# Performance work log

Hardware: AMD Instinct MI355X
Metric: run time of the kernel (lower is better)

## Reference

```python
import jax, jax.numpy as jnp
import numpy as np

M = 16
C = 7 * M          # 112, stage-8 channels
CLS = 20
TOPK = 3
NQ = 20000         # current-frame active sites at stage 8
NS = 8192          # support-frame active sites at stage 8
SCALE = 128.0      # voxel coordinate range at this depth


def setup_inputs() -> dict:
    key = jax.random.key(0)
    ks = jax.random.split(key, 9)
    coords_q = jax.random.uniform(ks[0], (NQ, 3), jnp.float32) * SCALE
    coords_s = jax.random.uniform(ks[1], (NS, 3), jnp.float32) * SCALE
    x7 = jax.random.normal(ks[2], (NQ, C), jnp.float32)
    feat_s7 = jax.random.normal(ks[3], (NS, C), jnp.float32)
    feat_s = jax.random.normal(ks[4], (NS, C), jnp.float32)
    w_attn = jax.random.normal(ks[5], (C,), jnp.float32) * 0.1
    W1 = jax.random.normal(ks[6], (2 * C, C), jnp.float32) * (1.0 / np.sqrt(2 * C))
    gamma = jnp.ones((C,), jnp.float32)
    beta = jnp.zeros((C,), jnp.float32)
    W2 = jax.random.normal(ks[7], (C, C), jnp.float32) * (1.0 / np.sqrt(C))
    W_cls = jax.random.normal(ks[8], (C, CLS), jnp.float32) * (1.0 / np.sqrt(C))
    b_cls = jnp.zeros((CLS,), jnp.float32)
    return dict(coords_q=coords_q, coords_s=coords_s, x7=x7, feat_s7=feat_s7,
                feat_s=feat_s, w_attn=w_attn, W1=W1, gamma=gamma, beta=beta,
                W2=W2, W_cls=W_cls, b_cls=b_cls)


def reference(coords_q, coords_s, x7, feat_s7, feat_s, w_attn, W1, gamma, beta, W2, W_cls, b_cls):
    # GlobalMeanAttentionPooling: attention-weighted mean over support sites -> global vector [C]
    a = jax.nn.softmax(feat_s7 @ w_attn)          # [NS]
    g = a @ feat_s7                                # [C]
    # GlobalMaskLayer: channel-wise sigmoid gating of current-frame features
    feat_q = x7 * jax.nn.sigmoid(g)                # [NQ, C]
    # DistMatchLayer_v4: top-3 nearest support voxels per query, softmax(-d2) weighting
    q2 = jnp.sum(coords_q * coords_q, -1, keepdims=True)   # [NQ, 1]
    s2 = jnp.sum(coords_s * coords_s, -1)                  # [NS]
    d2 = q2 + s2[None, :] - 2.0 * (coords_q @ coords_s.T)  # [NQ, NS]
    negd, idx = jax.lax.top_k(-d2, TOPK)                   # [NQ, K]
    w = jax.nn.softmax(negd, axis=-1)                      # [NQ, K]
    matched = jnp.einsum('nk,nkc->nc', w, feat_s[idx])     # [NQ, C]
    # tune_sub: 1x1 subconv (14m->7m) -> BN(eval affine) + ReLU -> 1x1 subconv (7m->7m)
    h = jnp.concatenate([feat_q, matched], -1) @ W1        # [NQ, C]
    h = jax.nn.relu(h * gamma + beta) @ W2                 # [NQ, C]
    # final classifier linear
    return h @ W_cls + b_cls                               # [NQ, CLS]
```

## Files before the change

### kernel.cpp

```cpp
#include <hip/hip_runtime.h>

#define NQv 20000
#define NSv 8192
#define Cv  112
#define CLSv 20
#define INFF 3.4e38f
#define JINF 0x7fffffff

#define GC 16
#define NCELL 4096
#define CELLH 8.0f
#define INVH 0.125f

#define POOLB 32
#define PT 256
#define PNW (POOLB * PT / 64)

#define SBLK (NQv / 4)
#define MB (NQv / 32)
#define WS_START 3616
#define WS_PTS4  5668
#define WS_W1TH  38440
#define WS_W1TL  50984
#define WS_W2TH  63528
#define WS_W2TL  70696
#define WS_WCT   77864

typedef __attribute__((ext_vector_type(8))) short bf16x8;
typedef __attribute__((ext_vector_type(4))) float f32x4;
typedef unsigned short us;

__device__ __forceinline__ float bf2f(us u) {
    union { unsigned int i; float f; } v; v.i = ((unsigned int)u) << 16; return v.f;
}
__device__ __forceinline__ us f2bf(float f) {
    union { float f; unsigned int i; } v; v.f = f;
    unsigned int r = v.i + 0x7fffu + ((v.i >> 16) & 1u);
    return (us)(r >> 16);
}
__device__ __forceinline__ void split(float v, us& h, us& l) {
    h = f2bf(v); l = f2bf(v - bf2f(h));
}

__global__ __launch_bounds__(PT) void k_prep(const float* __restrict__ cs,
                                             const float* __restrict__ fs7,
                                             const float* __restrict__ wat,
                                             const float* __restrict__ W1,
                                             const float* __restrict__ W2,
                                             const float* __restrict__ Wc,
                                             float* __restrict__ ws) {
    int b = blockIdx.x, tid = threadIdx.x;

    if (b == POOLB + 1) {
        us* w1h = (us*)(ws + WS_W1TH);
        us* w1l = (us*)(ws + WS_W1TL);
        for (int idx = tid; idx < Cv * 224; idx += PT) {
            int c = idx / 224, k = idx - c * 224;
            us h, l; split(W1[k * Cv + c], h, l);
            w1h[c * 224 + k] = h; w1l[c * 224 + k] = l;
        }
        return;
    }
    if (b == POOLB + 2) {
        us* w2h = (us*)(ws + WS_W2TH);
        us* w2l = (us*)(ws + WS_W2TL);
        for (int idx = tid; idx < Cv * 128; idx += PT) {
            int c = idx >> 7, k = idx & 127;
            float v = (k < Cv) ? W2[k * Cv + c] : 0.f;
            us h, l; split(v, h, l);
            w2h[c * 128 + k] = h; w2l[c * 128 + k] = l;
        }
        float* wct = ws + WS_WCT;
        for (int idx = tid; idx < CLSv * Cv; idx += PT) {
            int cls = idx / Cv, k = idx - cls * Cv;
            wct[cls * Cv + k] = Wc[k * CLSv + cls];
        }
        return;
    }
    if (b == POOLB) {
        __shared__ int cnt[NCELL];
        __shared__ int ssum[PT];
        us* startg = (us*)(ws + WS_START);
        float4* pts4 = (float4*)(ws + WS_PTS4);
        for (int i = tid; i < NCELL; i += PT) cnt[i] = 0;
        __syncthreads();
        for (int k = 0; k < NSv / PT; ++k) {
            int p = k * PT + tid;
            float x = cs[3 * p], y = cs[3 * p + 1], z = cs[3 * p + 2];
            int cx = (int)(x * INVH), cy = (int)(y * INVH), cz = (int)(z * INVH);
            cx = cx > 15 ? 15 : cx; cy = cy > 15 ? 15 : cy; cz = cz > 15 ? 15 : cz;
            atomicAdd(&cnt[(cz * GC + cy) * GC + cx], 1);
        }
        __syncthreads();
        int base = tid * 16, local = 0, c[16];
        #pragma unroll
        for (int i = 0; i < 16; ++i) { c[i] = cnt[base + i]; local += c[i]; }
        ssum[tid] = local;
        __syncthreads();
        for (int off = 1; off < PT; off <<= 1) {
            int v = (tid >= off) ? ssum[tid - off] : 0;
            __syncthreads();
            ssum[tid] += v;
            __syncthreads();
        }
        int run = ssum[tid] - local;
        #pragma unroll
        for (int i = 0; i < 16; ++i) {
            startg[base + i] = (us)run;
            cnt[base + i] = run;
            run += c[i];
        }
        if (tid == 0) startg[NCELL] = (us)NSv;
        __syncthreads();
        for (int k = 0; k < NSv / PT; ++k) {
            int p = k * PT + tid;
            float x = cs[3 * p], y = cs[3 * p + 1], z = cs[3 * p + 2];
            int cx = (int)(x * INVH), cy = (int)(y * INVH), cz = (int)(z * INVH);
            cx = cx > 15 ? 15 : cx; cy = cy > 15 ? 15 : cy; cz = cz > 15 ? 15 : cz;
            int slot = atomicAdd(&cnt[(cz * GC + cy) * GC + cx], 1);
            pts4[slot] = make_float4(-2.f * x, -2.f * y, -2.f * z, (float)p);
        }
        return;
    }

    __shared__ float red[PT / 64][Cv + 1];
    int gtid = b * PT + tid;
    int wid = gtid >> 6, lw = tid >> 6, lane = gtid & 63, l2 = lane * 2;
    float2 wa = make_float2(0.f, 0.f);
    if (lane < 56) wa = *(const float2*)(wat + l2);
    float gx = 0.f, gy = 0.f, z = 0.f;
    for (int g = 0; g < 8; ++g) {
        float2 f[8]; float part[8];
        #pragma unroll
        for (int u = 0; u < 8; ++u) {
            int i = wid + (g * 8 + u) * PNW;
            f[u] = (lane < 56) ? *(const float2*)(fs7 + i * Cv + l2) : make_float2(0.f, 0.f);
            part[u] = f[u].x * wa.x + f[u].y * wa.y;
        }
        #pragma unroll
        for (int off = 32; off; off >>= 1)
            #pragma unroll
            for (int u = 0; u < 8; ++u) part[u] += __shfl_xor(part[u], off, 64);
        #pragma unroll
        for (int u = 0; u < 8; ++u) {
            float p = __expf(part[u]);
            gx = fmaf(p, f[u].x, gx); gy = fmaf(p, f[u].y, gy); z += p;
        }
    }
    if (lane < 56) { red[lw][l2] = gx; red[lw][l2 + 1] = gy; }
    if (lane == 0) red[lw][Cv] = z;
    __syncthreads();
    if (tid < Cv + 1)
        ws[b * (Cv + 1) + tid] = red[0][tid] + red[1][tid] + red[2][tid] + red[3][tid];
}

__device__ __forceinline__ void scan_run(const float4* __restrict__ pts4,
                                         int a, int b, float qx, float qy, float qz,
                                         float& E0, float& E1, float& E2,
                                         int& J0, int& J1, int& J2) {
    for (int k = a; k < b; ++k) {
        float4 P = pts4[k];
        float x = -0.5f * P.x, y = -0.5f * P.y, z = -0.5f * P.z;
        float s2 = fmaf(x, x, fmaf(y, y, z * z));
        float e = fmaf(qx, P.x, fmaf(qy, P.y, fmaf(qz, P.z, s2)));
        int j = (int)P.w;
        bool lt2 = (e < E2) || (e == E2 && j < J2);
        if (lt2) {
            bool lt1 = (e < E1) || (e == E1 && j < J1);
            bool lt0 = (e < E0) || (e == E0 && j < J0);
            E2 = lt1 ? E1 : e;              J2 = lt1 ? J1 : j;
            E1 = lt0 ? E0 : (lt1 ? e : E1); J1 = lt0 ? J0 : (lt1 ? j : J1);
            if (lt0) { E0 = e; J0 = j; }
        }
    }
}

__global__ __launch_bounds__(256) void k_search(const float* __restrict__ cq,
                                                const float* __restrict__ ws,
                                                float* __restrict__ out) {
    const us* __restrict__ startg = (const us*)(ws + WS_START);
    const float4* __restrict__ pts4 = (const float4*)(ws + WS_PTS4);
    int tid = threadIdx.x, lane = tid & 63, widx = tid >> 6;
    int q = blockIdx.x * 4 + widx;
    float qx = cq[3 * q], qy = cq[3 * q + 1], qz = cq[3 * q + 2];
    float q2 = fmaf(qx, qx, fmaf(qy, qy, qz * qz));
    int cx = (int)(qx * INVH), cy = (int)(qy * INVH), cz = (int)(qz * INVH);
    cx = cx > 15 ? 15 : cx; cy = cy > 15 ? 15 : cy; cz = cz > 15 ? 15 : cz;
    float E0 = INFF, E1 = INFF, E2 = INFF;
    int   J0 = JINF, J1 = JINF, J2 = JINF;

    if (lane < 27) {
        int dz = lane / 9 - 1, dy = (lane / 3) % 3 - 1, dx = lane % 3 - 1;
        int xc = cx + dx, yc = cy + dy, zc = cz + dz;
        if ((unsigned)xc < 16u && (unsigned)yc < 16u && (unsigned)zc < 16u) {
            int cc = (zc * GC + yc) * GC + xc;
            scan_run(pts4, startg[cc], startg[cc + 1], qx, qy, qz, E0, E1, E2, J0, J1, J2);
        }
    }
    for (int s = 2; s <= 15; ++s) {
        float t0 = E0, t1 = E1, t2 = E2;
        #pragma unroll
        for (int off = 1; off < 64; off <<= 1) {
            float b0 = __shfl_xor(t0, off, 64);
            float b1 = __shfl_xor(t1, off, 64);
            float b2 = __shfl_xor(t2, off, 64);
            float xx = fmaxf(t0, b0), yy = fminf(t1, b1);
            float zz = fmaxf(t1, b1), uu = fminf(t2, b2);
            t0 = fminf(t0, b0);
            t1 = fminf(xx, yy);
            t2 = fminf(fminf(fmaxf(xx, yy), zz), uu);
        }
        int r = s - 1;
        int xl = cx - r > 0 ? cx - r : 0, xh = cx + r < 15 ? cx + r : 15;
        int yl = cy - r > 0 ? cy - r : 0, yh = cy + r < 15 ? cy + r : 15;
        int zl = cz - r > 0 ? cz - r : 0, zh = cz + r < 15 ? cz + r : 15;
        float fx = INFF, fy = INFF, fz = INFF;
        if (xl > 0)  fx = qx - xl * CELLH;
        if (xh < 15) fx = fminf(fx, (xh + 1) * CELLH - qx);
        if (yl > 0)  fy = qy - yl * CELLH;
        if (yh < 15) fy = fminf(fy, (yh + 1) * CELLH - qy);
        if (zl > 0)  fz = qz - zl * CELLH;
        if (zh < 15) fz = fminf(fz, (zh + 1) * CELLH - qz);
        float dmin = fminf(fx, fminf(fy, fz));
        if (dmin * dmin > t2 + q2 + 0.5f) break;

        int side = 2 * s + 1, s2n = side * side, tot = s2n * side;
        for (int idx = lane; idx < tot; idx += 64) {
            int dz = idx / s2n - s;
            int rem = idx - (dz + s) * s2n;
            int dy = rem / side - s;
            int dx = rem - (dy + s) * side - s;
            int ax = dx < 0 ? -dx : dx, ay = dy < 0 ? -dy : dy, az = dz < 0 ? -dz : dz;
            if (ax != s && ay != s && az != s) continue;
            int xc = cx + dx, yc = cy + dy, zc = cz + dz;
            if ((unsigned)xc > 15u || (unsigned)yc > 15u || (unsigned)zc > 15u) continue;
            int cc = (zc * GC + yc) * GC + xc;
            scan_run(pts4, startg[cc], startg[cc + 1], qx, qy, qz, E0, E1, E2, J0, J1, J2);
        }
    }
    float h0 = E0, h1 = E1, h2 = E2; int g0 = J0, g1 = J1, g2 = J2;
    float EF[3]; int JF[3];
    #pragma unroll
    for (int t = 0; t < 3; ++t) {
        float mv = h0; int mj = g0;
        #pragma unroll
        for (int off = 1; off < 64; off <<= 1) {
            float ov = __shfl_xor(mv, off, 64);
            int   oj = __shfl_xor(mj, off, 64);
            if (ov < mv || (ov == mv && oj < mj)) { mv = ov; mj = oj; }
        }
        EF[t] = mv; JF[t] = mj;
        bool win = (h0 == mv) && (g0 == mj);
        h0 = win ? h1 : h0; g0 = win ? g1 : g0;
        h1 = win ? h2 : h1; g1 = win ? g2 : g1;
        h2 = win ? INFF : h2; g2 = win ? JINF : g2;
    }
    if (lane == 0) {
        int A0 = (JF[0] < 0 || JF[0] >= NSv) ? 0 : JF[0];
        int A1 = (JF[1] < 0 || JF[1] >= NSv) ? 0 : JF[1];
        int A2 = (JF[2] < 0 || JF[2] >= NSv) ? 0 : JF[2];
        ((int*)out)[q * CLSv]     = A0 | (A1 << 16);
        ((int*)out)[q * CLSv + 1] = A2;
    }
}

__global__ __launch_bounds__(448) void k_mlp(
        const float* __restrict__ cq, const float* __restrict__ cs,
        const float* __restrict__ x7, const float* __restrict__ fs,
        const float* __restrict__ gma, const float* __restrict__ bta,
        const float* __restrict__ bc, const float* __restrict__ ws,
        float* __restrict__ out) {
    __shared__ __align__(16) us vbh[32 * 232];
    __shared__ __align__(16) us vbl[32 * 232];
    __shared__ __align__(16) us hbh[32 * 136];
    __shared__ __align__(16) us hbl[32 * 136];
    __shared__ __align__(16) float h2f[32 * 116];
    __shared__ float gate[Cv];
    __shared__ int   qi[32][3];
    __shared__ float qw[32][3];

    int tid = threadIdx.x;
    int q0 = blockIdx.x * 32;

    if (tid < Cv) {
        float st = 0.f, zt = 0.f;
        for (int b = 0; b < POOLB; ++b) {
            st += ws[b * (Cv + 1) + tid];
            zt += ws[b * (Cv + 1) + Cv];
        }
        gate[tid] = 1.0f / (1.0f + __expf(-(st / zt)));
    }
    int ut = tid - 128;
    if (ut >= 0 && ut < 32) {
        int q = q0 + ut;
        int A = ((const int*)out)[q * CLSv];
        int B = ((const int*)out)[q * CLSv + 1];
        int J0 = A & 0xFFFF, J1 = (A >> 16) & 0xFFFF, J2 = B;
        J0 = (J0 < 0 || J0 >= NSv) ? 0 : J0;
        J1 = (J1 < 0 || J1 >= NSv) ? 0 : J1;
        J2 = (J2 < 0 || J2 >= NSv) ? 0 : J2;
        float qx = cq[3 * q], qy = cq[3 * q + 1], qz = cq[3 * q + 2];
        float e[3]; int JJ[3] = {J0, J1, J2};
        #pragma unroll
        for (int r = 0; r < 3; ++r) {
            float x = cs[3 * JJ[r]], y = cs[3 * JJ[r] + 1], z = cs[3 * JJ[r] + 2];
            float s2 = fmaf(x, x, fmaf(y, y, z * z));
            e[r] = fmaf(qx, -2.f * x, fmaf(qy, -2.f * y, fmaf(qz, -2.f * z, s2)));
        }
        float w1v = __expf(e[0] - e[1]);
        float w2v = __expf(e[0] - e[2]);
        float iw  = 1.0f / (1.0f + w1v + w2v);
        qw[ut][0] = iw; qw[ut][1] = w1v * iw; qw[ut][2] = w2v * iw;
        qi[ut][0] = J0; qi[ut][1] = J1; qi[ut][2] = J2;
    }
    for (int i = tid; i < 32 * 16; i += 448) {
        int q = i >> 4, kk = Cv + (i & 15);
        hbh[q * 136 + kk] = 0; hbl[q * 136 + kk] = 0;
    }
    __syncthreads();

    {
        int vq = tid / 14, e = tid - vq * 14;
        int gq = q0 + vq;
        int k0 = e * 16;
        float vals[16];
        if (e < 7) {
            const float4* xr = (const float4*)(x7 + gq * Cv + k0);
            #pragma unroll
            for (int i = 0; i < 4; ++i) {
                float4 v = xr[i];
                vals[i * 4]     = v.x * gate[k0 + i * 4];
                vals[i * 4 + 1] = v.y * gate[k0 + i * 4 + 1];
                vals[i * 4 + 2] = v.z * gate[k0 + i * 4 + 2];
                vals[i * 4 + 3] = v.w * gate[k0 + i * 4 + 3];
            }
        } else {
            int kk = k0 - Cv;
            float w0 = qw[vq][0], w1v = qw[vq][1], w2v = qw[vq][2];
            const float4* r0 = (const float4*)(fs + qi[vq][0] * Cv + kk);
            const float4* r1 = (const float4*)(fs + qi[vq][1] * Cv + kk);
            const float4* r2 = (const float4*)(fs + qi[vq][2] * Cv + kk);
            #pragma unroll
            for (int i = 0; i < 4; ++i) {
                float4 a = r0[i], b = r1[i], c = r2[i];
                vals[i * 4]     = w0 * a.x + w1v * b.x + w2v * c.x;
                vals[i * 4 + 1] = w0 * a.y + w1v * b.y + w2v * c.y;
                vals[i * 4 + 2] = w0 * a.z + w1v * b.z + w2v * c.z;
                vals[i * 4 + 3] = w0 * a.w + w1v * b.w + w2v * c.w;
            }
        }
        #pragma unroll
        for (int i = 0; i < 16; ++i) {
            us h, l; split(vals[i], h, l);
            vbh[vq * 232 + k0 + i] = h;
            vbl[vq * 232 + k0 + i] = l;
        }
    }
    __syncthreads();

    int w = tid >> 6, lane = tid & 63, quad = lane >> 4, l16 = lane & 15;
    int cc = w * 16 + l16;

    {
        f32x4 acc0 = {0.f, 0.f, 0.f, 0.f};
        f32x4 acc1 = {0.f, 0.f, 0.f, 0.f};
        const us* w1h = (const us*)(ws + WS_W1TH) + cc * 224;
        const us* w1l = (const us*)(ws + WS_W1TL) + cc * 224;
        #pragma unroll
        for (int ks = 0; ks < 7; ++ks) {
            int ko = ks * 32 + quad * 8;
            bf16x8 bh  = *(const bf16x8*)(w1h + ko);
            bf16x8 bl  = *(const bf16x8*)(w1l + ko);
            bf16x8 a0h = *(const bf16x8*)(vbh + l16 * 232 + ko);
            bf16x8 a0l = *(const bf16x8*)(vbl + l16 * 232 + ko);
            bf16x8 a1h = *(const bf16x8*)(vbh + (l16 + 16) * 232 + ko);
            bf16x8 a1l = *(const bf16x8*)(vbl + (l16 + 16) * 232 + ko);
            acc0 = __builtin_amdgcn_mfma_f32_16x16x32_bf16(a0h, bh, acc0, 0, 0, 0);
            acc0 = __builtin_amdgcn_mfma_f32_16x16x32_bf16(a0l, bh, acc0, 0, 0, 0);
            acc0 = __builtin_amdgcn_mfma_f32_16x16x32_bf16(a0h, bl, acc0, 0, 0, 0);
            acc1 = __builtin_amdgcn_mfma_f32_16x16x32_bf16(a1h, bh, acc1, 0, 0, 0);
            acc1 = __builtin_amdgcn_mfma_f32_16x16x32_bf16(a1l, bh, acc1, 0, 0, 0);
            acc1 = __builtin_amdgcn_mfma_f32_16x16x32_bf16(a1h, bl, acc1, 0, 0, 0);
        }
        float g = gma[cc], bb = bta[cc];
        #pragma unroll
        for (int r = 0; r < 4; ++r) {
            int q = quad * 4 + r;
            float h = fmaf(acc0[r], g, bb); h = h > 0.f ? h : 0.f;
            us hh, ll; split(h, hh, ll);
            hbh[q * 136 + cc] = hh; hbl[q * 136 + cc] = ll;
            float h2 = fmaf(acc1[r], g, bb); h2 = h2 > 0.f ? h2 : 0.f;
            split(h2, hh, ll);
            hbh[(q + 16) * 136 + cc] = hh; hbl[(q + 16) * 136 + cc] = ll;
        }
    }
    __syncthreads();

    {
        f32x4 acc0 = {0.f, 0.f, 0.f, 0.f};
        f32x4 acc1 = {0.f, 0.f, 0.f, 0.f};
        const us* w2h = (const us*)(ws + WS_W2TH) + cc * 128;
        const us* w2l = (const us*)(ws + WS_W2TL) + cc * 128;
        #pragma unroll
        for (int ks = 0; ks < 4; ++ks) {
            int ko = ks * 32 + quad * 8;
            bf16x8 bh  = *(const bf16x8*)(w2h + ko);
            bf16x8 bl  = *(const bf16x8*)(w2l + ko);
            bf16x8 a0h = *(const bf16x8*)(hbh + l16 * 136 + ko);
            bf16x8 a0l = *(const bf16x8*)(hbl + l16 * 136 + ko);
            bf16x8 a1h = *(const bf16x8*)(hbh + (l16 + 16) * 136 + ko);
            bf16x8 a1l = *(const bf16x8*)(hbl + (l16 + 16) * 136 + ko);
            acc0 = __builtin_amdgcn_mfma_f32_16x16x32_bf16(a0h, bh, acc0, 0, 0, 0);
            acc0 = __builtin_amdgcn_mfma_f32_16x16x32_bf16(a0l, bh, acc0, 0, 0, 0);
            acc0 = __builtin_amdgcn_mfma_f32_16x16x32_bf16(a0h, bl, acc0, 0, 0, 0);
            acc1 = __builtin_amdgcn_mfma_f32_16x16x32_bf16(a1h, bh, acc1, 0, 0, 0);
            acc1 = __builtin_amdgcn_mfma_f32_16x16x32_bf16(a1l, bh, acc1, 0, 0, 0);
            acc1 = __builtin_amdgcn_mfma_f32_16x16x32_bf16(a1h, bl, acc1, 0, 0, 0);
        }
        #pragma unroll
        for (int r = 0; r < 4; ++r) {
            int q = quad * 4 + r;
            h2f[q * 116 + cc] = acc0[r];
            h2f[(q + 16) * 116 + cc] = acc1[r];
        }
    }
    __syncthreads();

    for (int it = tid; it < 32 * CLSv; it += 448) {
        int cls = it % CLSv, qq = it / CLSv;
        const float4* wr = (const float4*)(ws + WS_WCT + cls * Cv);
        const float4* hr = (const float4*)(h2f + qq * 116);
        float a = bc[cls];
        #pragma unroll 7
        for (int i = 0; i < 28; ++i) {
            float4 h = hr[i], v = wr[i];
            a = fmaf(h.x, v.x, fmaf(h.y, v.y, fmaf(h.z, v.z, fmaf(h.w, v.w, a))));
        }
        out[(q0 + qq) * CLSv + cls] = a;
    }
}

extern "C" void kernel_launch(void* const* d_in, const int* in_sizes, int n_in,
                              void* d_out, int out_size, void* d_ws, size_t ws_size,
                              hipStream_t stream) {
    const float* cq  = (const float*)d_in[0];
    const float* cs  = (const float*)d_in[1];
    const float* x7  = (const float*)d_in[2];
    const float* fs7 = (const float*)d_in[3];
    const float* fs  = (const float*)d_in[4];
    const float* wat = (const float*)d_in[5];
    const float* W1  = (const float*)d_in[6];
    const float* gma = (const float*)d_in[7];
    const float* bta = (const float*)d_in[8];
    const float* W2  = (const float*)d_in[9];
    const float* Wc  = (const float*)d_in[10];
    const float* bc  = (const float*)d_in[11];
    float* ws  = (float*)d_ws;
    float* out = (float*)d_out;

    k_prep<<<POOLB + 3, PT, 0, stream>>>(cs, fs7, wat, W1, W2, Wc, ws);
    k_search<<<SBLK, 256, 0, stream>>>(cq, ws, out);
    k_mlp<<<MB, 448, 0, stream>>>(cq, cs, x7, fs, gma, bta, bc, ws, out);
}
```

Baseline: 157.3 us.

## Merge kNN top-3 keys into 64-bit reductions and widen prep blocks to 1024 threads

The kNN search now packs each (distance, index) pair into an order-preserving 64-bit key. A single butterfly merge of top-3 per ring then gives both the pruning bound and the final indices, which replaces the separate three-pass argmin reduction at the end. The prep kernel runs 1024 threads per block, so the pooling loop shrinks to 2 groups and the grid build uses a wave-shuffle scan instead of the barrier-heavy shared-memory scan. The trade-off is 64-bit shuffles in every ring iteration, at roughly twice the cost of the float shuffles, and higher register pressure in the larger prep blocks.

```diff
diff --git a/kernel.cpp b/kernel.cpp
--- a/kernel.cpp
+++ b/kernel.cpp
@@ -13,7 +13,7 @@
 #define INVH 0.125f
 
 #define POOLB 32
-#define PT 256
+#define PT 1024
 #define PNW (POOLB * PT / 64)
 
 #define SBLK (NQv / 4)
@@ -29,6 +29,7 @@
 typedef __attribute__((ext_vector_type(8))) short bf16x8;
 typedef __attribute__((ext_vector_type(4))) float f32x4;
 typedef unsigned short us;
+typedef unsigned long long u64;
 
 __device__ __forceinline__ float bf2f(us u) {
     union { unsigned int i; float f; } v; v.i = ((unsigned int)u) << 16; return v.f;
@@ -41,6 +42,19 @@
 __device__ __forceinline__ void split(float v, us& h, us& l) {
     h = f2bf(v); l = f2bf(v - bf2f(h));
 }
+
+__device__ __forceinline__ u64 mkkey(float e, int j) {
+    union { float f; unsigned int i; } v; v.f = e;
+    unsigned int ue = v.i ^ ((unsigned int)((int)v.i >> 31) | 0x80000000u);
+    return ((u64)ue << 32) | (unsigned int)j;
+}
+__device__ __forceinline__ float keyval(u64 k) {
+    unsigned int ue = (unsigned int)(k >> 32);
+    unsigned int u = ue ^ ((unsigned int)((int)(~ue) >> 31) | 0x80000000u);
+    union { unsigned int i; float f; } v; v.i = u; return v.f;
+}
+__device__ __forceinline__ u64 umin64(u64 a, u64 b) { return a < b ? a : b; }
+__device__ __forceinline__ u64 umax64(u64 a, u64 b) { return a > b ? a : b; }
 
 __global__ __launch_bounds__(PT) void k_prep(const float* __restrict__ cs,
                                              const float* __restrict__ fs7,
@@ -79,46 +93,57 @@
     }
     if (b == POOLB) {
         __shared__ int cnt[NCELL];
-        __shared__ int ssum[PT];
+        __shared__ int wsum[PT / 64];
         us* startg = (us*)(ws + WS_START);
         float4* pts4 = (float4*)(ws + WS_PTS4);
+        int lane = tid & 63, wv = tid >> 6;
         for (int i = tid; i < NCELL; i += PT) cnt[i] = 0;
         __syncthreads();
+        float xx[8], yy[8], zz[8]; int cid[8]; int pp[8];
+        #pragma unroll
         for (int k = 0; k < NSv / PT; ++k) {
             int p = k * PT + tid;
-            float x = cs[3 * p], y = cs[3 * p + 1], z = cs[3 * p + 2];
-            int cx = (int)(x * INVH), cy = (int)(y * INVH), cz = (int)(z * INVH);
+            pp[k] = p;
+            xx[k] = cs[3 * p]; yy[k] = cs[3 * p + 1]; zz[k] = cs[3 * p + 2];
+            int cx = (int)(xx[k] * INVH), cy = (int)(yy[k] * INVH), cz = (int)(zz[k] * INVH);
             cx = cx > 15 ? 15 : cx; cy = cy > 15 ? 15 : cy; cz = cz > 15 ? 15 : cz;
-            atomicAdd(&cnt[(cz * GC + cy) * GC + cx], 1);
+            cid[k] = (cz * GC + cy) * GC + cx;
+            atomicAdd(&cnt[cid[k]], 1);
         }
         __syncthreads();
-        int base = tid * 16, local = 0, c[16];
-        #pragma unroll
-        for (int i = 0; i < 16; ++i) { c[i] = cnt[base + i]; local += c[i]; }
-        ssum[tid] = local;
+        int base = tid * 4;
+        int c0 = cnt[base], c1 = cnt[base + 1], c2 = cnt[base + 2], c3 = cnt[base + 3];
+        int local = c0 + c1 + c2 + c3;
+        int inc = local;
+        #pragma unroll
+        for (int off = 1; off < 64; off <<= 1) {
+            int v = __shfl_up(inc, off, 64);
+            if (lane >= off) inc += v;
+        }
+        if (lane == 63) wsum[wv] = inc;
         __syncthreads();
-        for (int off = 1; off < PT; off <<= 1) {
-            int v = (tid >= off) ? ssum[tid - off] : 0;
-            __syncthreads();
-            ssum[tid] += v;
-            __syncthreads();
-        }
-        int run = ssum[tid] - local;
-        #pragma unroll
-        for (int i = 0; i < 16; ++i) {
-            startg[base + i] = (us)run;
-            cnt[base + i] = run;
-            run += c[i];
-        }
+        if (tid < PT / 64) {
+            int v = wsum[tid];
+            #pragma unroll
+            for (int off = 1; off < 16; off <<= 1) {
+                int o = __shfl_up(v, off, 64);
+                if (tid >= off) v += o;
+            }
+            wsum[tid] = v;
+        }
+        __syncthreads();
+        int wbase = (wv == 0) ? 0 : wsum[wv - 1];
+        int run = wbase + inc - local;
+        startg[base] = (us)run;     cnt[base] = run;     run += c0;
+        startg[base + 1] = (us)run; cnt[base + 1] = run; run += c1;
+        startg[base + 2] = (us)run; cnt[base + 2] = run; run += c2;
+        startg[base + 3] = (us)run; cnt[base + 3] = run;
         if (tid == 0) startg[NCELL] = (us)NSv;
         __syncthreads();
+        #pragma unroll
         for (int k = 0; k < NSv / PT; ++k) {
-            int p = k * PT + tid;
-            float x = cs[3 * p], y = cs[3 * p + 1], z = cs[3 * p + 2];
-            int cx = (int)(x * INVH), cy = (int)(y * INVH), cz = (int)(z * INVH);
-            cx = cx > 15 ? 15 : cx; cy = cy > 15 ? 15 : cy; cz = cz > 15 ? 15 : cz;
-            int slot = atomicAdd(&cnt[(cz * GC + cy) * GC + cx], 1);
-            pts4[slot] = make_float4(-2.f * x, -2.f * y, -2.f * z, (float)p);
+            int slot = atomicAdd(&cnt[cid[k]], 1);
+            pts4[slot] = make_float4(-2.f * xx[k], -2.f * yy[k], -2.f * zz[k], (float)pp[k]);
         }
         return;
     }
@@ -129,7 +154,7 @@
     float2 wa = make_float2(0.f, 0.f);
     if (lane < 56) wa = *(const float2*)(wat + l2);
     float gx = 0.f, gy = 0.f, z = 0.f;
-    for (int g = 0; g < 8; ++g) {
+    for (int g = 0; g < 2; ++g) {
         float2 f[8]; float part[8];
         #pragma unroll
         for (int u = 0; u < 8; ++u) {
@@ -150,8 +175,12 @@
     if (lane < 56) { red[lw][l2] = gx; red[lw][l2 + 1] = gy; }
     if (lane == 0) red[lw][Cv] = z;
     __syncthreads();
-    if (tid < Cv + 1)
-        ws[b * (Cv + 1) + tid] = red[0][tid] + red[1][tid] + red[2][tid] + red[3][tid];
+    if (tid < Cv + 1) {
+        float s = 0.f;
+        #pragma unroll
+        for (int i = 0; i < PT / 64; ++i) s += red[i][tid];
+        ws[b * (Cv + 1) + tid] = s;
+    }
 }
 
 __device__ __forceinline__ void scan_run(const float4* __restrict__ pts4,
@@ -197,19 +226,24 @@
             scan_run(pts4, startg[cc], startg[cc + 1], qx, qy, qz, E0, E1, E2, J0, J1, J2);
         }
     }
-    for (int s = 2; s <= 15; ++s) {
-        float t0 = E0, t1 = E1, t2 = E2;
+
+    u64 K0, K1, K2;
+    for (int s = 2; ; ++s) {
+        K0 = mkkey(E0, J0); K1 = mkkey(E1, J1); K2 = mkkey(E2, J2);
         #pragma unroll
         for (int off = 1; off < 64; off <<= 1) {
-            float b0 = __shfl_xor(t0, off, 64);
-            float b1 = __shfl_xor(t1, off, 64);
-            float b2 = __shfl_xor(t2, off, 64);
-            float xx = fmaxf(t0, b0), yy = fminf(t1, b1);
-            float zz = fmaxf(t1, b1), uu = fminf(t2, b2);
-            t0 = fminf(t0, b0);
-            t1 = fminf(xx, yy);
-            t2 = fminf(fminf(fmaxf(xx, yy), zz), uu);
-        }
+            u64 b0 = __shfl_xor(K0, off, 64);
+            u64 b1 = __shfl_xor(K1, off, 64);
+            u64 b2 = __shfl_xor(K2, off, 64);
+            u64 xx = umax64(K0, b0), yy = umin64(K1, b1);
+            u64 zz = umax64(K1, b1), uu = umin64(K2, b2);
+            K0 = umin64(K0, b0);
+            u64 n1 = umin64(xx, yy);
+            K2 = umin64(umin64(umax64(xx, yy), zz), uu);
+            K1 = n1;
+        }
+        if (s > 15) break;
+
         int r = s - 1;
         int xl = cx - r > 0 ? cx - r : 0, xh = cx + r < 15 ? cx + r : 15;
         int yl = cy - r > 0 ? cy - r : 0, yh = cy + r < 15 ? cy + r : 15;
@@ -222,6 +256,7 @@
         if (zl > 0)  fz = qz - zl * CELLH;
         if (zh < 15) fz = fminf(fz, (zh + 1) * CELLH - qz);
         float dmin = fminf(fx, fminf(fy, fz));
+        float t2 = keyval(K2);
         if (dmin * dmin > t2 + q2 + 0.5f) break;
 
         int side = 2 * s + 1, s2n = side * side, tot = s2n * side;
@@ -238,29 +273,15 @@
             scan_run(pts4, startg[cc], startg[cc + 1], qx, qy, qz, E0, E1, E2, J0, J1, J2);
         }
     }
-    float h0 = E0, h1 = E1, h2 = E2; int g0 = J0, g1 = J1, g2 = J2;
-    float EF[3]; int JF[3];
-    #pragma unroll
-    for (int t = 0; t < 3; ++t) {
-        float mv = h0; int mj = g0;
-        #pragma unroll
-        for (int off = 1; off < 64; off <<= 1) {
-            float ov = __shfl_xor(mv, off, 64);
-            int   oj = __shfl_xor(mj, off, 64);
-            if (ov < mv || (ov == mv && oj < mj)) { mv = ov; mj = oj; }
-        }
-        EF[t] = mv; JF[t] = mj;
-        bool win = (h0 == mv) && (g0 == mj);
-        h0 = win ? h1 : h0; g0 = win ? g1 : g0;
-        h1 = win ? h2 : h1; g1 = win ? g2 : g1;
-        h2 = win ? INFF : h2; g2 = win ? JINF : g2;
-    }
     if (lane == 0) {
-        int A0 = (JF[0] < 0 || JF[0] >= NSv) ? 0 : JF[0];
-        int A1 = (JF[1] < 0 || JF[1] >= NSv) ? 0 : JF[1];
-        int A2 = (JF[2] < 0 || JF[2] >= NSv) ? 0 : JF[2];
-        ((int*)out)[q * CLSv]     = A0 | (A1 << 16);
-        ((int*)out)[q * CLSv + 1] = A2;
+        unsigned int A0 = (unsigned int)K0;
+        unsigned int A1 = (unsigned int)K1;
+        unsigned int A2 = (unsigned int)K2;
+        if (A0 >= NSv) A0 = 0;
+        if (A1 >= NSv) A1 = 0;
+        if (A2 >= NSv) A2 = 0;
+        ((int*)out)[q * CLSv]     = (int)(A0 | (A1 << 16));
+        ((int*)out)[q * CLSv + 1] = (int)A2;
     }
 }
 
```

Result: no change. 154.6 us (-1.7%).
